# Kernel optimization log

Hardware: AMD Instinct MI355X
Metric: run time of the kernel (lower is better)

The kernel has to match this reference:

```python
import jax, jax.numpy as jnp
import numpy as np

B, H, W, C = 64, 56, 56, 192
HEADS, WS, SS, MLP = 6, 7, 3, 768
N = WS * WS            # 49 tokens per window
NW = (H // WS) * (W // WS)  # 64 windows per image
HEAD_DIM = C // HEADS
SCALE = HEAD_DIM ** (-0.5)


def _rpi(ws):
    # relative position index, (N, N) int
    coords = np.stack(np.meshgrid(np.arange(ws), np.arange(ws), indexing='ij')).reshape(2, -1)
    rel = (coords[:, :, None] - coords[:, None, :]).transpose(1, 2, 0)
    rel[:, :, 0] += ws - 1
    rel[:, :, 1] += ws - 1
    rel[:, :, 0] *= 2 * ws - 1
    return rel.sum(-1)

RPI = _rpi(WS).reshape(-1)  # (N*N,)


def _attn_mask():
    # additive shift mask, (NW, N, N)
    label = np.zeros((H, W))
    cnt = 0
    slices = (slice(0, -WS), slice(-WS, -SS), slice(-SS, None))
    for hs in slices:
        for ws_ in slices:
            label[hs, ws_] = cnt
            cnt += 1
    lab = label.reshape(H // WS, WS, W // WS, WS).transpose(0, 2, 1, 3).reshape(NW, N)
    diff = lab[:, None, :] - lab[:, :, None]
    return np.where(diff != 0, -100.0, 0.0).astype(np.float32)

MASK = jnp.asarray(_attn_mask())  # (NW, N, N)


def _ln(t, g, b, eps=1e-5):
    m = jnp.mean(t, -1, keepdims=True)
    v = jnp.mean((t - m) ** 2, -1, keepdims=True)
    return (t - m) * jax.lax.rsqrt(v + eps) * g + b


def setup_inputs() -> dict:
    key = jax.random.key(0)
    ks = jax.random.split(key, 6)
    s = 0.02
    return {
        'x': jax.random.normal(ks[0], (B, H * W, C), jnp.float32),
        'ln1_g': jnp.ones((C,), jnp.float32),
        'ln1_b': jnp.zeros((C,), jnp.float32),
        'qkv_w': jax.random.normal(ks[1], (C, 3 * C), jnp.float32) * s,
        'qkv_b': jnp.zeros((3 * C,), jnp.float32),
        'proj_w': jax.random.normal(ks[2], (C, C), jnp.float32) * s,
        'proj_b': jnp.zeros((C,), jnp.float32),
        'rpb': jax.random.normal(ks[3], ((2 * WS - 1) ** 2, HEADS), jnp.float32) * s,
        'ln2_g': jnp.ones((C,), jnp.float32),
        'ln2_b': jnp.zeros((C,), jnp.float32),
        'mlp_w1': jax.random.normal(ks[4], (C, MLP), jnp.float32) * s,
        'mlp_b1': jnp.zeros((MLP,), jnp.float32),
        'mlp_w2': jax.random.normal(ks[5], (MLP, C), jnp.float32) * s,
        'mlp_b2': jnp.zeros((C,), jnp.float32),
    }


def reference(x, ln1_g, ln1_b, qkv_w, qkv_b, proj_w, proj_b, rpb,
              ln2_g, ln2_b, mlp_w1, mlp_b1, mlp_w2, mlp_b2):
    # ---- Residual(PreNorm(Swin(WindowAttention))) ----
    h = _ln(x, ln1_g, ln1_b)                       # (B, L, C)
    h = h.reshape(B, H, W, C)
    h = jnp.roll(h, (-SS, -SS), (1, 2))            # cyclic shift
    # window partition -> (B*NW, N, C)
    h = h.reshape(B, H // WS, WS, W // WS, WS, C).transpose(0, 1, 3, 2, 4, 5).reshape(-1, N, C)
    qkv = (h @ qkv_w + qkv_b).reshape(-1, N, 3, HEADS, HEAD_DIM).transpose(2, 0, 3, 1, 4)
    q, k, v = qkv[0] * SCALE, qkv[1], qkv[2]       # (B*NW, heads, N, d)
    attn = jnp.einsum('bhid,bhjd->bhij', q, k)     # (B*NW, heads, N, N)
    bias = rpb[RPI].reshape(N, N, HEADS).transpose(2, 0, 1)  # (heads, N, N)
    attn = attn + bias[None]
    attn = attn.reshape(B, NW, HEADS, N, N) + MASK[None, :, None]
    attn = jax.nn.softmax(attn.reshape(-1, HEADS, N, N), axis=-1)
    out = jnp.einsum('bhij,bhjd->bhid', attn, v).transpose(0, 2, 1, 3).reshape(-1, N, C)
    out = out @ proj_w + proj_b
    # window reverse -> (B, H, W, C)
    out = out.reshape(B, H // WS, W // WS, WS, WS, C).transpose(0, 1, 3, 2, 4, 5).reshape(B, H, W, C)
    out = jnp.roll(out, (SS, SS), (1, 2)).reshape(B, H * W, C)
    x = x + out
    # ---- Residual(PreNorm(Mlp)) ----
    h2 = _ln(x, ln2_g, ln2_b)
    h2 = jax.nn.gelu(h2 @ mlp_w1 + mlp_b1, approximate=False) @ mlp_w2 + mlp_b2
    return x + h2
```

## Files before the change

### kernel.cpp

```cpp
#include <hip/hip_runtime.h>
#include <math.h>

typedef __attribute__((ext_vector_type(8))) short short8;
typedef __attribute__((ext_vector_type(4))) float floatx4;

#define M_TOT 200704
#define SCALE_Q 0.17677669529663687f

__device__ __forceinline__ float u2f(unsigned int u){ return __uint_as_float(u << 16); }
__device__ __forceinline__ unsigned short f2u(float f){
  unsigned int x = __float_as_uint(f);
  x += 0x7fffu + ((x >> 16) & 1u);
  return (unsigned short)(x >> 16);
}

#define GLD16(gp, lp) __builtin_amdgcn_global_load_lds( \
    (const __attribute__((address_space(1))) void*)(gp), \
    (__attribute__((address_space(3))) void*)(lp), 16, 0, 0)

__device__ __forceinline__ int win_to_x(int m){
  int bb = m / 3136; int rem = m - bb*3136;
  int w = rem / 49, n = rem - w*49;
  int wh = w >> 3, ww = w & 7;
  int i = n / 7, j = n - i*7;
  int p = wh*7 + i + 3; if (p >= 56) p -= 56;
  int q = ww*7 + j + 3; if (q >= 56) q -= 56;
  return bb*3136 + p*56 + q;
}

__global__ void conv_wt(const float* __restrict__ in, unsigned short* __restrict__ out,
                        int K, int N){
  int t = blockIdx.x*256 + threadIdx.x;
  if (t < K*N){ int n = t / K, k = t - n*K; out[t] = f2u(in[k*N + n]); }
}
__global__ void rowmap_k(int* __restrict__ map){
  int t = blockIdx.x*256 + threadIdx.x;
  if (t < M_TOT) map[t] = win_to_x(t);
}
__global__ void bm_k(const float* __restrict__ rpb, unsigned short* __restrict__ BM){
  int w = blockIdx.x / 6, h = blockIdx.x - (blockIdx.x/6)*6;
  int t = threadIdx.x;
  unsigned short* o = BM + ((size_t)blockIdx.x << 12);
  int wh = w >> 3, ww = w & 7;
  for (int z = 0; z < 16; ++z){
    int idx = t*16 + z;
    int i = idx >> 6, j = idx & 63;
    float val = -30000.0f;
    if (i < 49 && j < 49){
      int yi = i/7, xi = i - (i/7)*7, yj = j/7, xj = j - (j/7)*7;
      int pi_ = wh*7 + yi, qi_ = ww*7 + xi;
      int pj_ = wh*7 + yj, qj_ = ww*7 + xj;
      int li = (pi_<49?0:(pi_<53?1:2))*3 + (qi_<49?0:(qi_<53?1:2));
      int lj = (pj_<49?0:(pj_<53?1:2))*3 + (qj_<49?0:(qj_<53?1:2));
      int rel = (yi-yj+6)*13 + (xi-xj+6);
      val = rpb[rel*6 + h] + ((li == lj) ? 0.0f : -100.0f);
    }
    o[idx] = f2u(val);
  }
}

template<int KTOT, int NCG, int LNMODE, int EPI>
__global__ __launch_bounds__(512, 4) void gemm_kernel(
    const void* __restrict__ A, int astride, long row0g,
    const unsigned short* __restrict__ Wt,
    const float* __restrict__ lng, const float* __restrict__ lnb,
    const float* __restrict__ bias, const float* __restrict__ res,
    void* __restrict__ outp, int ostride, const int* __restrict__ rowmap){
  constexpr bool AFULL = (KTOT == 192);
  constexpr int AROW  = AFULL ? 192 : 64;
  constexpr int NCH   = KTOT / 64;
  __shared__ __align__(16) unsigned short As[AFULL ? 128*192 : 128*64];
  __shared__ __align__(16) unsigned short Ws[192*64];
  int tid = threadIdx.x;
  int gx = gridDim.x;
  int nwg = gx * gridDim.y;
  int orig = blockIdx.y * gx + blockIdx.x;
  int qc = nwg >> 3, rc = nwg & 7;
  int xcd = orig & 7, idxk = orig >> 3;
  int wgid = (xcd < rc ? xcd*(qc+1) : rc*(qc+1) + (xcd-rc)*qc) + idxk;
  int bx = wgid % gx, by = wgid / gx;
  long lrow0 = (long)by * 128;
  int lane = tid & 63, wv = tid >> 6;
  int rw = wv >> 2, cw = wv & 3;
  int quad = lane >> 4, l16 = lane & 15;

  if constexpr (LNMODE != 0){
    int rr = tid >> 2, sub = tid & 3;
    long srow = (LNMODE == 1) ? (long)rowmap[row0g + lrow0 + rr] : (row0g + lrow0 + rr);
    const float* rp = (const float*)A + srow*192 + sub*48;
    float va[48];
    float s = 0.f, q2 = 0.f;
    #pragma unroll
    for (int i = 0; i < 12; ++i){
      float4 f = *(const float4*)(rp + i*4);
      va[i*4+0] = f.x; va[i*4+1] = f.y; va[i*4+2] = f.z; va[i*4+3] = f.w;
      s += (f.x + f.y) + (f.z + f.w);
      q2 = fmaf(f.x, f.x, q2); q2 = fmaf(f.y, f.y, q2);
      q2 = fmaf(f.z, f.z, q2); q2 = fmaf(f.w, f.w, q2);
    }
    s  += __shfl_xor(s, 1);  q2 += __shfl_xor(q2, 1);
    s  += __shfl_xor(s, 2);  q2 += __shfl_xor(q2, 2);
    float mean = s*(1.f/192.f);
    float rs = rsqrtf(q2*(1.f/192.f) - mean*mean + 1e-5f);
    float mrs = mean * rs;
    unsigned short* dstb = As + rr*192;
    #pragma unroll
    for (int i = 0; i < 12; ++i){
      float4 g4 = *(const float4*)(lng + sub*48 + i*4);
      float4 b4 = *(const float4*)(lnb + sub*48 + i*4);
      ushort4 o;
      o.x = f2u(fmaf(fmaf(va[i*4+0], rs, -mrs), g4.x, b4.x));
      o.y = f2u(fmaf(fmaf(va[i*4+1], rs, -mrs), g4.y, b4.y));
      o.z = f2u(fmaf(fmaf(va[i*4+2], rs, -mrs), g4.z, b4.z));
      o.w = f2u(fmaf(fmaf(va[i*4+3], rs, -mrs), g4.w, b4.w));
      *(ushort4*)(dstb + (((sub*6 + (i>>1)) ^ (rr&7))<<3) + ((i&1)<<2)) = o;
    }
  } else if constexpr (AFULL){
    #pragma unroll
    for (int it = 0; it < 6; ++it){
      int gi = (wv*6 + it)*64 + lane;
      int r = gi / 24, g = gi - r*24;
      const unsigned short* src = (const unsigned short*)A
          + (lrow0 + r)*(long)astride + ((g ^ (r&7))<<3);
      GLD16(src, As + ((wv*6 + it)<<9));
    }
  }

  #pragma unroll
  for (int g = 0; g < NCG; ++g){
    int n0 = (bx*NCG + g) * 192;
    floatx4 acc[12];
    #pragma unroll
    for (int i = 0; i < 12; ++i) acc[i] = (floatx4){0.f,0.f,0.f,0.f};

    for (int c = 0; c < NCH; ++c){
      if (g || c) __syncthreads();
      if constexpr (!AFULL){
        #pragma unroll
        for (int it = 0; it < 2; ++it){
          int gi = (wv*2 + it)*64 + lane;
          int r = gi >> 3, gg = gi & 7;
          const unsigned short* src = (const unsigned short*)A
              + (lrow0 + r)*(long)astride + c*64 + ((gg ^ (r&7))<<3);
          GLD16(src, As + ((wv*2 + it)<<9));
        }
      }
      #pragma unroll
      for (int it = 0; it < 3; ++it){
        int gi = (wv*3 + it)*64 + lane;
        int r = gi >> 3, gg = gi & 7;
        const unsigned short* src = Wt + (long)(n0 + r)*KTOT + c*64 + ((gg ^ (r&7))<<3);
        GLD16(src, Ws + ((wv*3 + it)<<9));
      }
      __syncthreads();
      int gA0 = AFULL ? c*8 : 0;
      #pragma unroll
      for (int kk = 0; kk < 2; ++kk){
        int ga = gA0 + kk*4 + quad;
        short8 af[4];
        #pragma unroll
        for (int m = 0; m < 4; ++m){
          int r = rw*64 + m*16 + l16;
          af[m] = *(const short8*)(As + r*AROW + ((ga ^ (r&7))<<3));
        }
        int gb = kk*4 + quad;
        #pragma unroll
        for (int n = 0; n < 3; ++n){
          int rb = cw*48 + n*16 + l16;
          short8 bf = *(const short8*)(Ws + rb*64 + ((gb ^ (rb&7))<<3));
          #pragma unroll
          for (int m = 0; m < 4; ++m)
            acc[m*3+n] = __builtin_amdgcn_mfma_f32_16x16x32_bf16(af[m], bf, acc[m*3+n], 0, 0, 0);
        }
      }
    }

    #pragma unroll
    for (int m = 0; m < 4; ++m){
      #pragma unroll
      for (int r2 = 0; r2 < 4; ++r2){
        long lm = lrow0 + rw*64 + m*16 + quad*4 + r2;
        long drow = 0;
        if (EPI == 1) drow = rowmap[row0g + lm];
        if (EPI == 3) drow = row0g + lm;
        #pragma unroll
        for (int n = 0; n < 3; ++n){
          int col = n0 + cw*48 + n*16 + l16;
          float v = acc[m*3+n][r2] + bias[col];
          if (EPI == 0){
            if (col < 192) v *= SCALE_Q;
            ((unsigned short*)outp)[lm*(long)ostride + col] = f2u(v);
          } else if (EPI == 1){
            v += res[drow*192 + col];
            ((float*)outp)[drow*192 + col] = v;
          } else if (EPI == 2){
            float zz = 1.5957691216057308f * v * fmaf(v*v, 0.044715f, 1.0f);
            v = v * __builtin_amdgcn_rcpf(1.0f + __expf(-zz));
            ((unsigned short*)outp)[lm*(long)ostride + col] = f2u(v);
          } else {
            v += res[drow*192 + col];
            ((float*)outp)[drow*192 + col] = v;
          }
        }
      }
    }
  }
}

__global__ __launch_bounds__(64) void attn_kernel(unsigned short* __restrict__ qkv,
    const unsigned short* __restrict__ BM, long win0g){
  __shared__ __align__(16) unsigned short Vt[32*64];
  __shared__ __align__(16) unsigned short Pl[64*72];
  int bid = blockIdx.x;
  int wb = bid / 6, head = bid - wb*6;
  int t = threadIdx.x;
  int q = t >> 4, l16 = t & 15;
  long base = (long)wb * 49 * 576;
  const unsigned short* qkvb = qkv + base;

  #pragma unroll
  for (int z = 0; z < 8; ++z){
    int idx = t + z*64;
    int d = idx >> 4, jz = 48 + (idx & 15);
    Vt[d*64 + ((((jz>>3) ^ (d&7))<<3) | (jz&7))] = 0;
  }
  for (int idx = t; idx < 784; idx += 64){
    int j = idx >> 4, d2 = (idx & 15)*2;
    unsigned int u = *(const unsigned int*)(qkvb + (long)j*576 + 384 + head*32 + d2);
    Vt[d2*64 + ((((j>>3) ^ (d2&7))<<3) | (j&7))]       = (unsigned short)(u & 0xffffu);
    Vt[(d2+1)*64 + ((((j>>3) ^ ((d2+1)&7))<<3) | (j&7))] = (unsigned short)(u >> 16);
  }

  short8 kf[4], qf[4];
  #pragma unroll
  for (int jt = 0; jt < 4; ++jt){
    int j = jt*16 + l16; j = j > 48 ? 48 : j;
    kf[jt] = *(const short8*)(qkvb + (long)j*576 + 192 + head*32 + q*8);
  }
  #pragma unroll
  for (int it = 0; it < 4; ++it){
    int i = it*16 + l16; i = i > 48 ? 48 : i;
    qf[it] = *(const short8*)(qkvb + (long)i*576 + head*32 + q*8);
  }
  floatx4 acc[16];
  #pragma unroll
  for (int z = 0; z < 16; ++z) acc[z] = (floatx4){0.f,0.f,0.f,0.f};
  #pragma unroll
  for (int jt = 0; jt < 4; ++jt){
    #pragma unroll
    for (int it = 0; it < 4; ++it)
      acc[jt*4+it] = __builtin_amdgcn_mfma_f32_16x16x32_bf16(kf[jt], qf[it], acc[jt*4+it], 0, 0, 0);
  }

  int w = (int)((win0g + wb) & 63);
  const unsigned short* bmp = BM + ((size_t)(w*6 + head) << 12);
  #pragma unroll
  for (int it = 0; it < 4; ++it){
    float mx = -3.0e38f;
    #pragma unroll
    for (int jt = 0; jt < 4; ++jt){
      ushort4 bm = *(const ushort4*)(bmp + (it*16 + l16)*64 + jt*16 + q*4);
      floatx4 s = acc[jt*4+it];
      s[0] += u2f(bm.x); s[1] += u2f(bm.y); s[2] += u2f(bm.z); s[3] += u2f(bm.w);
      acc[jt*4+it] = s;
      mx = fmaxf(mx, fmaxf(fmaxf(s[0], s[1]), fmaxf(s[2], s[3])));
    }
    mx = fmaxf(mx, __shfl_xor(mx, 16));
    mx = fmaxf(mx, __shfl_xor(mx, 32));
    float sum = 0.f;
    #pragma unroll
    for (int jt = 0; jt < 4; ++jt){
      floatx4 s = acc[jt*4+it];
      s[0] = __expf(s[0]-mx); s[1] = __expf(s[1]-mx);
      s[2] = __expf(s[2]-mx); s[3] = __expf(s[3]-mx);
      acc[jt*4+it] = s;
      sum += (s[0]+s[1]) + (s[2]+s[3]);
    }
    sum += __shfl_xor(sum, 16);
    sum += __shfl_xor(sum, 32);
    float inv = 1.0f / sum;
    #pragma unroll
    for (int jt = 0; jt < 4; ++jt){
      floatx4 s = acc[jt*4+it];
      ushort4 pk;
      pk.x = f2u(s[0]*inv); pk.y = f2u(s[1]*inv);
      pk.z = f2u(s[2]*inv); pk.w = f2u(s[3]*inv);
      *(ushort4*)(Pl + (it*16 + l16)*72 + jt*16 + q*4) = pk;
    }
  }
  __syncthreads();

  floatx4 oa[8];
  #pragma unroll
  for (int z = 0; z < 8; ++z) oa[z] = (floatx4){0.f,0.f,0.f,0.f};
  #pragma unroll
  for (int ks = 0; ks < 2; ++ks){
    short8 pf[4];
    #pragma unroll
    for (int mt = 0; mt < 4; ++mt)
      pf[mt] = *(const short8*)(Pl + (mt*16 + l16)*72 + ks*32 + q*8);
    #pragma unroll
    for (int nt = 0; nt < 2; ++nt){
      int d = nt*16 + l16;
      short8 vf = *(const short8*)(Vt + d*64 + (((ks*4 + q) ^ (d&7))<<3));
      #pragma unroll
      for (int mt = 0; mt < 4; ++mt)
        oa[mt*2+nt] = __builtin_amdgcn_mfma_f32_16x16x32_bf16(pf[mt], vf, oa[mt*2+nt], 0, 0, 0);
    }
  }
  #pragma unroll
  for (int mt = 0; mt < 4; ++mt){
    #pragma unroll
    for (int r = 0; r < 4; ++r){
      int i = mt*16 + q*4 + r;
      if (i < 49){
        unsigned short* op = qkv + base + (long)i*576 + head*32;
        op[l16]      = f2u(oa[mt*2+0][r]);
        op[16 + l16] = f2u(oa[mt*2+1][r]);
      }
    }
  }
}

extern "C" void kernel_launch(void* const* d_in, const int* in_sizes, int n_in,
                              void* d_out, int out_size, void* d_ws, size_t ws_size,
                              hipStream_t stream){
  const float* x     = (const float*)d_in[0];
  const float* ln1_g = (const float*)d_in[1];
  const float* ln1_b = (const float*)d_in[2];
  const float* qkv_w = (const float*)d_in[3];
  const float* qkv_b = (const float*)d_in[4];
  const float* proj_w= (const float*)d_in[5];
  const float* proj_b= (const float*)d_in[6];
  const float* rpb   = (const float*)d_in[7];
  const float* ln2_g = (const float*)d_in[8];
  const float* ln2_b = (const float*)d_in[9];
  const float* w1    = (const float*)d_in[10];
  const float* b1    = (const float*)d_in[11];
  const float* w2    = (const float*)d_in[12];
  const float* b2    = (const float*)d_in[13];
  float* out = (float*)d_out;

  unsigned short* wt_qkv  = (unsigned short*)d_ws;
  unsigned short* wt_proj = wt_qkv  + 576*192;
  unsigned short* wt_m1   = wt_proj + 192*192;
  unsigned short* wt_m2   = wt_m1   + 768*192;
  int* rowmap = (int*)(wt_m2 + 192*768);
  unsigned short* bm = (unsigned short*)(rowmap + M_TOT);
  unsigned short* buf = bm + (size_t)384*4096;
  size_t ovh = (size_t)(576*192 + 192*192 + 768*192 + 192*768)*2 + (size_t)M_TOT*4
             + (size_t)384*4096*2;
  size_t bufb = ws_size > ovh ? ws_size - ovh : 0;

  int da = 64;
  while (da > 2 && (size_t)3136*(size_t)da*1152ULL > bufb) da >>= 1;
  long Sa = 3136L*da;
  int nA = 64/da;
  static const long smlist[] = {200704,100352,50176,25088,12544,6272,1792,1024,512,256,128};
  long Sm = 128;
  for (int i = 0; i < 11; ++i) if ((size_t)smlist[i]*1536ULL <= bufb){ Sm = smlist[i]; break; }
  int nM = (int)(M_TOT / Sm);

  conv_wt<<<(192*576+255)/256, 256, 0, stream>>>(qkv_w, wt_qkv, 192, 576);
  conv_wt<<<(192*192+255)/256, 256, 0, stream>>>(proj_w, wt_proj, 192, 192);
  conv_wt<<<(192*768+255)/256, 256, 0, stream>>>(w1, wt_m1, 192, 768);
  conv_wt<<<(768*192+255)/256, 256, 0, stream>>>(w2, wt_m2, 768, 192);
  rowmap_k<<<(M_TOT+255)/256, 256, 0, stream>>>(rowmap);
  bm_k<<<384, 256, 0, stream>>>(rpb, bm);

  for (int s = 0; s < nA; ++s){
    long r0 = (long)s*Sa;
    gemm_kernel<192,3,1,0><<<dim3(1, Sa/128), 512, 0, stream>>>(
        x, 192, r0, wt_qkv, ln1_g, ln1_b, qkv_b, nullptr, buf, 576, rowmap);
    attn_kernel<<<(int)(Sa/49)*6, 64, 0, stream>>>(buf, bm, r0/49);
    gemm_kernel<192,1,0,1><<<dim3(1, Sa/128), 512, 0, stream>>>(
        buf, 576, r0, wt_proj, nullptr, nullptr, proj_b, x, out, 192, rowmap);
  }

  for (int s = 0; s < nM; ++s){
    long r0 = (long)s*Sm;
    gemm_kernel<192,2,2,2><<<dim3(2, Sm/128), 512, 0, stream>>>(
        out, 192, r0, wt_m1, ln2_g, ln2_b, b1, nullptr, buf, 768, rowmap);
    gemm_kernel<768,1,0,3><<<dim3(1, Sm/128), 512, 0, stream>>>(
        buf, 768, r0, wt_m2, nullptr, nullptr, b2, out, out, 192, rowmap);
  }
}
```

Before: 931.2 us.

## Double-buffer GEMM LDS tiles with K-chunk 32 and prefetch next chunk

Restructures the GEMM main loop to use 32-wide K chunks held in two LDS buffers. The next chunk's A/W tiles are prefetched via global_load_lds while MFMAs run on the current one, so there is one barrier per chunk instead of two. It also adds a new XOR swizzle for the 32-wide rows and raises launch-bounds occupancy to 6 for non-LN variants. The GELU is rewritten with exp2f and a folded constant. Smaller chunks mean more barriers and loop iterations, and the occupancy hint may force register spills.

```diff
diff --git a/kernel.cpp b/kernel.cpp
--- a/kernel.cpp
+++ b/kernel.cpp
@@ -17,6 +17,8 @@
 #define GLD16(gp, lp) __builtin_amdgcn_global_load_lds( \
     (const __attribute__((address_space(1))) void*)(gp), \
     (__attribute__((address_space(3))) void*)(lp), 16, 0, 0)
+
+__device__ __forceinline__ int sw32(int r, int g){ return g ^ ((r ^ (r >> 2)) & 3); }
 
 __device__ __forceinline__ int win_to_x(int m){
   int bb = m / 3136; int rem = m - bb*3136;
@@ -60,17 +62,16 @@
 }
 
 template<int KTOT, int NCG, int LNMODE, int EPI>
-__global__ __launch_bounds__(512, 4) void gemm_kernel(
+__global__ __launch_bounds__(512, LNMODE ? 4 : 6) void gemm_kernel(
     const void* __restrict__ A, int astride, long row0g,
     const unsigned short* __restrict__ Wt,
     const float* __restrict__ lng, const float* __restrict__ lnb,
     const float* __restrict__ bias, const float* __restrict__ res,
     void* __restrict__ outp, int ostride, const int* __restrict__ rowmap){
-  constexpr bool AFULL = (KTOT == 192);
-  constexpr int AROW  = AFULL ? 192 : 64;
-  constexpr int NCH   = KTOT / 64;
-  __shared__ __align__(16) unsigned short As[AFULL ? 128*192 : 128*64];
-  __shared__ __align__(16) unsigned short Ws[192*64];
+  constexpr bool AFULL = (LNMODE != 0);
+  constexpr int NCH = KTOT / 32;
+  __shared__ __align__(16) unsigned short As[AFULL ? 128*192 : 2*128*32];
+  __shared__ __align__(16) unsigned short Ws[2*192*32];
   int tid = threadIdx.x;
   int gx = gridDim.x;
   int nwg = gx * gridDim.y;
@@ -84,6 +85,29 @@
   int rw = wv >> 2, cw = wv & 3;
   int quad = lane >> 4, l16 = lane & 15;
 
+  auto stage_w = [&](int gg, int cc, int h){
+    int n0s = (bx*NCG + gg) * 192;
+    unsigned short* dst = Ws + h*(192*32);
+    {
+      int gi = wv*64 + lane;
+      int r = gi >> 2, g = gi & 3;
+      GLD16(Wt + (long)(n0s + r)*KTOT + cc*32 + (sw32(r,g)<<3), dst + (wv<<9));
+    }
+    if (wv < 4){
+      int idx = 8 + wv;
+      int gi = idx*64 + lane;
+      int r = gi >> 2, g = gi & 3;
+      GLD16(Wt + (long)(n0s + r)*KTOT + cc*32 + (sw32(r,g)<<3), dst + (idx<<9));
+    }
+  };
+  auto stage_a = [&](int cc, int h){
+    unsigned short* dst = As + h*(128*32);
+    int gi = wv*64 + lane;
+    int r = gi >> 2, g = gi & 3;
+    GLD16((const unsigned short*)A + (lrow0 + r)*(long)astride + cc*32 + (sw32(r,g)<<3),
+          dst + (wv<<9));
+  };
+
   if constexpr (LNMODE != 0){
     int rr = tid >> 2, sub = tid & 3;
     long srow = (LNMODE == 1) ? (long)rowmap[row0g + lrow0 + rr] : (row0g + lrow0 + rr);
@@ -115,17 +139,13 @@
       o.w = f2u(fmaf(fmaf(va[i*4+3], rs, -mrs), g4.w, b4.w));
       *(ushort4*)(dstb + (((sub*6 + (i>>1)) ^ (rr&7))<<3) + ((i&1)<<2)) = o;
     }
-  } else if constexpr (AFULL){
-    #pragma unroll
-    for (int it = 0; it < 6; ++it){
-      int gi = (wv*6 + it)*64 + lane;
-      int r = gi / 24, g = gi - r*24;
-      const unsigned short* src = (const unsigned short*)A
-          + (lrow0 + r)*(long)astride + ((g ^ (r&7))<<3);
-      GLD16(src, As + ((wv*6 + it)<<9));
-    }
-  }
-
+  } else {
+    stage_a(0, 0);
+  }
+  stage_w(0, 0, 0);
+  __syncthreads();
+
+  int cur = 0;
   #pragma unroll
   for (int g = 0; g < NCG; ++g){
     int n0 = (bx*NCG + g) * 192;
@@ -134,45 +154,38 @@
     for (int i = 0; i < 12; ++i) acc[i] = (floatx4){0.f,0.f,0.f,0.f};
 
     for (int c = 0; c < NCH; ++c){
-      if (g || c) __syncthreads();
-      if constexpr (!AFULL){
-        #pragma unroll
-        for (int it = 0; it < 2; ++it){
-          int gi = (wv*2 + it)*64 + lane;
-          int r = gi >> 3, gg = gi & 7;
-          const unsigned short* src = (const unsigned short*)A
-              + (lrow0 + r)*(long)astride + c*64 + ((gg ^ (r&7))<<3);
-          GLD16(src, As + ((wv*2 + it)<<9));
-        }
+      int cn = c + 1, gn = g;
+      if (cn == NCH){ cn = 0; gn = g + 1; }
+      if (gn < NCG){
+        if constexpr (!AFULL) stage_a(cn, cur ^ 1);
+        stage_w(gn, cn, cur ^ 1);
       }
-      #pragma unroll
-      for (int it = 0; it < 3; ++it){
-        int gi = (wv*3 + it)*64 + lane;
-        int r = gi >> 3, gg = gi & 7;
-        const unsigned short* src = Wt + (long)(n0 + r)*KTOT + c*64 + ((gg ^ (r&7))<<3);
-        GLD16(src, Ws + ((wv*3 + it)<<9));
-      }
-      __syncthreads();
-      int gA0 = AFULL ? c*8 : 0;
-      #pragma unroll
-      for (int kk = 0; kk < 2; ++kk){
-        int ga = gA0 + kk*4 + quad;
-        short8 af[4];
+      short8 af[4];
+      if constexpr (AFULL){
         #pragma unroll
         for (int m = 0; m < 4; ++m){
           int r = rw*64 + m*16 + l16;
-          af[m] = *(const short8*)(As + r*AROW + ((ga ^ (r&7))<<3));
+          af[m] = *(const short8*)(As + r*192 + (((c*4 + quad) ^ (r&7))<<3));
         }
-        int gb = kk*4 + quad;
+      } else {
+        const unsigned short* Ac = As + cur*(128*32);
         #pragma unroll
-        for (int n = 0; n < 3; ++n){
-          int rb = cw*48 + n*16 + l16;
-          short8 bf = *(const short8*)(Ws + rb*64 + ((gb ^ (rb&7))<<3));
-          #pragma unroll
-          for (int m = 0; m < 4; ++m)
-            acc[m*3+n] = __builtin_amdgcn_mfma_f32_16x16x32_bf16(af[m], bf, acc[m*3+n], 0, 0, 0);
+        for (int m = 0; m < 4; ++m){
+          int r = rw*64 + m*16 + l16;
+          af[m] = *(const short8*)(Ac + r*32 + (sw32(r,quad)<<3));
         }
       }
+      const unsigned short* Wc = Ws + cur*(192*32);
+      #pragma unroll
+      for (int n = 0; n < 3; ++n){
+        int rb = cw*48 + n*16 + l16;
+        short8 bf = *(const short8*)(Wc + rb*32 + (sw32(rb,quad)<<3));
+        #pragma unroll
+        for (int m = 0; m < 4; ++m)
+          acc[m*3+n] = __builtin_amdgcn_mfma_f32_16x16x32_bf16(af[m], bf, acc[m*3+n], 0, 0, 0);
+      }
+      __syncthreads();
+      cur ^= 1;
     }
 
     #pragma unroll
@@ -194,8 +207,8 @@
             v += res[drow*192 + col];
             ((float*)outp)[drow*192 + col] = v;
           } else if (EPI == 2){
-            float zz = 1.5957691216057308f * v * fmaf(v*v, 0.044715f, 1.0f);
-            v = v * __builtin_amdgcn_rcpf(1.0f + __expf(-zz));
+            float z2 = -2.3022082f * v * fmaf(v*v, 0.044715f, 1.0f);
+            v = v * __builtin_amdgcn_rcpf(1.0f + exp2f(z2));
             ((unsigned short*)outp)[lm*(long)ostride + col] = f2u(v);
           } else {
             v += res[drow*192 + col];
```

New measurement: 1.074 ms. 1.15x slower.
